# Performance work log

Hardware: AMD Instinct MI355X
Metric: run time of the kernel (lower is better)

Reference implementation:

```python
import jax, jax.numpy as jnp
import numpy as np
from jax import lax

L, H, C, V, BLK = 6, 12, 768, 50257, 1024
B, T = 4, 1024
HD = C // H
EPS = 1e-5


def _norm(key, shape, scale=0.02):
    return jax.random.normal(key, shape, dtype=jnp.float32) * scale


def setup_inputs() -> dict:
    key = jax.random.key(0)
    ks = jax.random.split(key, 16)
    idx = jax.random.randint(ks[0], (B, T), 0, V)
    inp = {
        "idx": idx,
        "wte": _norm(ks[1], (V, C)),
        "wpe": _norm(ks[2], (BLK, C)),
        "ln1_s": jnp.ones((L, C)),
        "ln1_b": jnp.zeros((L, C)),
        "qkv_w": _norm(ks[3], (L, C, 3 * C)),
        "qkv_b": jnp.zeros((L, 3 * C)),
        "proj_w": _norm(ks[4], (L, C, C)),
        "proj_b": jnp.zeros((L, C)),
        "ln2_s": jnp.ones((L, C)),
        "ln2_b": jnp.zeros((L, C)),
        "fc_w": _norm(ks[5], (L, C, 4 * C)),
        "fc_b": jnp.zeros((L, 4 * C)),
        "fcp_w": _norm(ks[6], (L, 4 * C, C)),
        "fcp_b": jnp.zeros((L, C)),
        "lnf_s": jnp.ones((C,)),
        "lnf_b": jnp.zeros((C,)),
    }
    return inp


def layer_norm(x, s, b):
    mu = jnp.mean(x, axis=-1, keepdims=True)
    var = jnp.mean(jnp.square(x - mu), axis=-1, keepdims=True)
    return (x - mu) * lax.rsqrt(var + EPS) * s + b


def block(x, p):
    ln1_s, ln1_b, qkv_w, qkv_b, proj_w, proj_b, ln2_s, ln2_b, fc_w, fc_b, fcp_w, fcp_b = p
    Bx, Tx, Cx = x.shape
    h = layer_norm(x, ln1_s, ln1_b)
    qkv = h @ qkv_w + qkv_b  # [B,T,3C]
    q, k, v = jnp.split(qkv, 3, axis=-1)
    q = q.reshape(Bx, Tx, H, HD).swapaxes(1, 2)  # [B,H,T,hd]
    k = k.reshape(Bx, Tx, H, HD).swapaxes(1, 2)
    v = v.reshape(Bx, Tx, H, HD).swapaxes(1, 2)
    attn = jnp.einsum("bhqd,bhkd->bhqk", q, k) / jnp.sqrt(jnp.float32(HD))
    mask = jnp.tril(jnp.ones((Tx, Tx), dtype=bool))
    attn = jnp.where(mask, attn, -jnp.inf)
    attn = jax.nn.softmax(attn, axis=-1)
    y = jnp.einsum("bhqk,bhkd->bhqd", attn, v)
    y = y.swapaxes(1, 2).reshape(Bx, Tx, Cx)
    x = x + (y @ proj_w + proj_b)
    h = layer_norm(x, ln2_s, ln2_b)
    h = jax.nn.gelu(h @ fc_w + fc_b, approximate=True)
    x = x + (h @ fcp_w + fcp_b)
    return x


def reference(idx, wte, wpe, ln1_s, ln1_b, qkv_w, qkv_b, proj_w, proj_b,
              ln2_s, ln2_b, fc_w, fc_b, fcp_w, fcp_b, lnf_s, lnf_b):
    Tx = idx.shape[1]
    x = wte[idx] + wpe[:Tx][None]  # [B,T,C]
    params = (ln1_s, ln1_b, qkv_w, qkv_b, proj_w, proj_b,
              ln2_s, ln2_b, fc_w, fc_b, fcp_w, fcp_b)
    def step(carry, p):
        return block(carry, p), None
    x, _ = lax.scan(step, x, params)
    x = layer_norm(x, lnf_s, lnf_b)
    logits = x @ wte.T  # tied embedding attend
    return logits
```

## Files before the change

kernel.cpp:

```cpp
#include <hip/hip_runtime.h>
#include <math.h>

#define LNUM 6
#define HNUM 12
#define CDIM 768
#define VDIM 50257
#define BDIM 4
#define TDIM 1024
#define NTOK 4096

typedef __bf16 bf16;
typedef __bf16 bf16x8 __attribute__((ext_vector_type(8)));
typedef float  floatx4 __attribute__((ext_vector_type(4)));
typedef unsigned int u32;

__device__ inline void gload16(const bf16* gsrc, bf16* lds) {
  __builtin_amdgcn_global_load_lds(
      (const __attribute__((address_space(1))) u32*)gsrc,
      (__attribute__((address_space(3))) u32*)lds, 16, 0, 0);
}

__global__ void k_cvt_bf16(const float* __restrict__ in, bf16* __restrict__ out, long n) {
  long i = ((long)blockIdx.x * blockDim.x + threadIdx.x) * 4;
  long stride = (long)gridDim.x * blockDim.x * 4;
  for (; i < n; i += stride) {
    float4 v = *reinterpret_cast<const float4*>(in + i);
    bf16 b0 = (bf16)v.x, b1 = (bf16)v.y, b2 = (bf16)v.z, b3 = (bf16)v.w;
    ushort4 pk;
    pk.x = __builtin_bit_cast(unsigned short, b0);
    pk.y = __builtin_bit_cast(unsigned short, b1);
    pk.z = __builtin_bit_cast(unsigned short, b2);
    pk.w = __builtin_bit_cast(unsigned short, b3);
    *reinterpret_cast<ushort4*>(out + i) = pk;
  }
}

__global__ void k_transpose_cvt(const float* __restrict__ in, bf16* __restrict__ out, int K, int N) {
  __shared__ float tile[32][33];
  int n0 = blockIdx.x * 32, k0 = blockIdx.y * 32;
  int nx = threadIdx.x & 31, ty = threadIdx.x >> 5;
  #pragma unroll
  for (int p = 0; p < 4; ++p) {
    int k = ty + p * 8;
    tile[k][nx] = in[(size_t)(k0 + k) * N + n0 + nx];
  }
  __syncthreads();
  #pragma unroll
  for (int p = 0; p < 4; ++p) {
    int n = ty + p * 8;
    out[(size_t)(n0 + n) * K + k0 + nx] = (bf16)tile[nx][n];
  }
}

__global__ void k_embed(const int* __restrict__ idx, const float* __restrict__ wte,
                        const float* __restrict__ wpe, float* __restrict__ x) {
  int tok = blockIdx.x;
  int t = tok & (TDIM - 1);
  int id = idx[tok];
  const float* a = wte + (size_t)id * CDIM;
  const float* p = wpe + (size_t)t * CDIM;
  float* o = x + (size_t)tok * CDIM;
  for (int c = threadIdx.x; c < CDIM; c += 256) o[c] = a[c] + p[c];
}

__global__ __launch_bounds__(256) void k_layernorm(const float* __restrict__ x,
    const float* __restrict__ sc, const float* __restrict__ bi, bf16* __restrict__ out) {
  __shared__ float red[8];
  int row = blockIdx.x;
  const float* xr = x + (size_t)row * CDIM;
  int t = threadIdx.x;
  float v0 = xr[t], v1 = xr[t + 256], v2 = xr[t + 512];
  float s = v0 + v1 + v2;
  #pragma unroll
  for (int o = 32; o > 0; o >>= 1) s += __shfl_down(s, o);
  if ((t & 63) == 0) red[t >> 6] = s;
  __syncthreads();
  float mean = (red[0] + red[1] + red[2] + red[3]) * (1.0f / CDIM);
  float d0 = v0 - mean, d1 = v1 - mean, d2 = v2 - mean;
  float q = d0 * d0 + d1 * d1 + d2 * d2;
  #pragma unroll
  for (int o = 32; o > 0; o >>= 1) q += __shfl_down(q, o);
  if ((t & 63) == 0) red[4 + (t >> 6)] = q;
  __syncthreads();
  float var = (red[4] + red[5] + red[6] + red[7]) * (1.0f / CDIM);
  float rs = rsqrtf(var + 1e-5f);
  bf16* orow = out + (size_t)row * CDIM;
  orow[t]       = (bf16)(d0 * rs * sc[t]       + bi[t]);
  orow[t + 256] = (bf16)(d1 * rs * sc[t + 256] + bi[t + 256]);
  orow[t + 512] = (bf16)(d2 * rs * sc[t + 512] + bi[t + 512]);
}

__device__ inline float gelu_f(float x) {
  float x3 = x * x * x;
  return 0.5f * x * (1.0f + tanhf(0.7978845608028654f * (x + 0.044715f * x3)));
}

template<int EPI>
__global__ __launch_bounds__(512, 1) void k_gemm8(
    const bf16* __restrict__ A, const bf16* __restrict__ Bt,
    const float* __restrict__ bias,
    float* __restrict__ Cf, bf16* __restrict__ Cb,
    int N, int K) {
  __shared__ __align__(16) bf16 lds[2][4][8192];
  const int nwg = gridDim.x;
  const int id = blockIdx.x;
  const int swz = (id & 7) * (nwg >> 3) + (id >> 3);
  const int m0 = (swz & 15) * 256;
  const int n0 = (swz >> 4) * 256;
  const int tid = threadIdx.x, lane = tid & 63, wave = tid >> 6;
  const int wr = wave >> 2, wc = wave & 3;
  const int g = lane >> 4, r16 = lane & 15;
  const int numK = K >> 6;

  const int srow = wave * 16 + (lane >> 2);
  const int scol = (lane & 3) * 8;
  const bf16* aptr0 = A  + (size_t)(m0 + srow) * K + scol;
  const bf16* aptr1 = A  + (size_t)(m0 + srow + 128) * K + scol;
  const bf16* bptr0 = Bt + (size_t)(n0 + srow) * K + scol;
  const bf16* bptr1 = Bt + (size_t)(n0 + srow + 128) * K + scol;
  const int a_off = (wr * 128 + r16) * 32 + g * 8;
  const int b_off = (wc * 64 + r16) * 32 + g * 8;

  floatx4 acc[8][4] = {};

#define STAGE_HALF(H) do {                                                \
    int H_ = (H);                                                         \
    if (H_ < numK * 4) {                                                  \
      int tau_ = H_ >> 2, h_ = H_ & 3;                                    \
      int isA_ = (h_ & 1), kk_ = (h_ >> 1) & 1;                           \
      bf16* dst_ = &lds[tau_ & 1][h_][wave * 512];                        \
      int ko_ = tau_ * 64 + kk_ * 32;                                     \
      gload16((isA_ ? aptr0 : bptr0) + ko_, dst_);                        \
      gload16((isA_ ? aptr1 : bptr1) + ko_, dst_ + 4096);                 \
    } } while (0)

  STAGE_HALF(0); STAGE_HALF(1); STAGE_HALF(2); STAGE_HALF(3);
  STAGE_HALF(4); STAGE_HALF(5); STAGE_HALF(6);
  asm volatile("s_waitcnt vmcnt(6)" ::: "memory");
  __builtin_amdgcn_s_barrier();

  for (int t = 0; t < numK; ++t) {
    const int p = t & 1;
    const int Hb = 4 * t + 7;
    bf16x8 af[4], bfr[4];

    #pragma unroll
    for (int j = 0; j < 4; ++j) bfr[j] = *(const bf16x8*)&lds[p][0][b_off + j * 512];
    #pragma unroll
    for (int i = 0; i < 4; ++i) af[i] = *(const bf16x8*)&lds[p][1][a_off + i * 512];
    STAGE_HALF(Hb);
    __builtin_amdgcn_s_barrier();
    asm volatile("s_waitcnt lgkmcnt(0)" ::: "memory");
    __builtin_amdgcn_s_setprio(1);
    #pragma unroll
    for (int i = 0; i < 4; ++i)
      #pragma unroll
      for (int j = 0; j < 4; ++j)
        acc[i][j] = __builtin_amdgcn_mfma_f32_16x16x32_bf16(af[i], bfr[j], acc[i][j], 0, 0, 0);
    __builtin_amdgcn_s_setprio(0);
    __builtin_amdgcn_s_barrier();

    #pragma unroll
    for (int i = 0; i < 4; ++i) af[i] = *(const bf16x8*)&lds[p][1][a_off + (i + 4) * 512];
    STAGE_HALF(Hb + 1);
    __builtin_amdgcn_s_barrier();
    asm volatile("s_waitcnt lgkmcnt(0)" ::: "memory");
    __builtin_amdgcn_s_setprio(1);
    #pragma unroll
    for (int i = 0; i < 4; ++i)
      #pragma unroll
      for (int j = 0; j < 4; ++j)
        acc[i + 4][j] = __builtin_amdgcn_mfma_f32_16x16x32_bf16(af[i], bfr[j], acc[i + 4][j], 0, 0, 0);
    __builtin_amdgcn_s_setprio(0);
    __builtin_amdgcn_s_barrier();

    #pragma unroll
    for (int j = 0; j < 4; ++j) bfr[j] = *(const bf16x8*)&lds[p][2][b_off + j * 512];
    #pragma unroll
    for (int i = 0; i < 4; ++i) af[i] = *(const bf16x8*)&lds[p][3][a_off + i * 512];
    STAGE_HALF(Hb + 2);
    __builtin_amdgcn_s_barrier();
    asm volatile("s_waitcnt lgkmcnt(0)" ::: "memory");
    __builtin_amdgcn_s_setprio(1);
    #pragma unroll
    for (int i = 0; i < 4; ++i)
      #pragma unroll
      for (int j = 0; j < 4; ++j)
        acc[i][j] = __builtin_amdgcn_mfma_f32_16x16x32_bf16(af[i], bfr[j], acc[i][j], 0, 0, 0);
    __builtin_amdgcn_s_setprio(0);
    __builtin_amdgcn_s_barrier();

    #pragma unroll
    for (int i = 0; i < 4; ++i) af[i] = *(const bf16x8*)&lds[p][3][a_off + (i + 4) * 512];
    STAGE_HALF(Hb + 3);
    __builtin_amdgcn_s_barrier();
    asm volatile("s_waitcnt lgkmcnt(0)" ::: "memory");
    __builtin_amdgcn_s_setprio(1);
    #pragma unroll
    for (int i = 0; i < 4; ++i)
      #pragma unroll
      for (int j = 0; j < 4; ++j)
        acc[i + 4][j] = __builtin_amdgcn_mfma_f32_16x16x32_bf16(af[i], bfr[j], acc[i + 4][j], 0, 0, 0);
    __builtin_amdgcn_s_setprio(0);
    if (t + 2 < numK) { asm volatile("s_waitcnt vmcnt(6)" ::: "memory"); }
    else              { asm volatile("s_waitcnt vmcnt(0)" ::: "memory"); }
    __builtin_amdgcn_s_barrier();
  }
#undef STAGE_HALF

  const int mb = m0 + wr * 128 + g * 4;
  const int nb = n0 + wc * 64 + r16;
  #pragma unroll
  for (int nf = 0; nf < 4; ++nf) {
    int n = nb + nf * 16;
    if (EPI == 0 && n >= N) continue;
    float bv = (EPI >= 3) ? bias[n] : 0.0f;
    #pragma unroll
    for (int mf = 0; mf < 8; ++mf) {
      #pragma unroll
      for (int q = 0; q < 4; ++q) {
        int m = mb + mf * 16 + q;
        float v = acc[mf][nf][q] + bv;
        size_t o = (size_t)m * N + n;
        if (EPI == 3)      Cb[o] = (bf16)gelu_f(v);
        else if (EPI == 4) Cb[o] = (bf16)v;
        else               Cf[o] = v;
      }
    }
  }
}

template<int TBM, int MI, int NI, int EPI>
__global__ __launch_bounds__(256) void k_gemm(
    const bf16* __restrict__ A, const bf16* __restrict__ Bt,
    const float* __restrict__ bias, const float* __restrict__ resid,
    float* __restrict__ Cf, bf16* __restrict__ Cb,
    int M, int N, int K) {
  constexpr int BN = 128;
  constexpr int WGN = BN / (NI * 16);
  constexpr int AI = TBM / 32;
  constexpr int BI = BN / 32;
  __shared__ __align__(16) bf16 As[TBM * 64];
  __shared__ __align__(16) bf16 Bs[BN * 64];
  const int m0 = blockIdx.x * TBM, n0 = blockIdx.y * BN;
  const int tid = threadIdx.x;
  const int lane = tid & 63, wave = tid >> 6;
  const int wr = wave / WGN, wc = wave % WGN;
  const int l8 = lane >> 3, s8 = lane & 7;
  const int g = lane >> 4, r16 = lane & 15;

  floatx4 acc[MI][NI] = {};

  const bf16* a_src = A + (size_t)(m0 + l8) * K + s8 * 8;
  const bf16* b_src = Bt + (size_t)(n0 + l8) * K + s8 * 8;

  for (int k0 = 0; k0 < K; k0 += 64) {
    #pragma unroll
    for (int t = 0; t < AI; ++t) {
      int row0 = wave * (TBM / 4) + t * 8;
      gload16(a_src + (size_t)row0 * K + k0, &As[row0 * 64]);
    }
    #pragma unroll
    for (int t = 0; t < BI; ++t) {
      int row0 = wave * 32 + t * 8;
      gload16(b_src + (size_t)row0 * K + k0, &Bs[row0 * 64]);
    }
    __syncthreads();
    #pragma unroll
    for (int kk = 0; kk < 2; ++kk) {
      bf16x8 af[MI], bfr[NI];
      #pragma unroll
      for (int i = 0; i < MI; ++i)
        af[i] = *reinterpret_cast<const bf16x8*>(&As[(wr * MI * 16 + i * 16 + r16) * 64 + g * 8 + kk * 32]);
      #pragma unroll
      for (int j = 0; j < NI; ++j)
        bfr[j] = *reinterpret_cast<const bf16x8*>(&Bs[(wc * NI * 16 + j * 16 + r16) * 64 + g * 8 + kk * 32]);
      #pragma unroll
      for (int i = 0; i < MI; ++i) {
        #pragma unroll
        for (int j = 0; j < NI; ++j)
          acc[i][j] = __builtin_amdgcn_mfma_f32_16x16x32_bf16(af[i], bfr[j], acc[i][j], 0, 0, 0);
      }
    }
    __syncthreads();
  }

  int mb = m0 + wr * MI * 16 + g * 4;
  int nb = n0 + wc * NI * 16 + r16;
  #pragma unroll
  for (int j = 0; j < NI; ++j) {
    int n = nb + j * 16;
    if (n >= N) continue;
    float bv = (EPI >= 2) ? bias[n] : 0.0f;
    #pragma unroll
    for (int i = 0; i < MI; ++i) {
      #pragma unroll
      for (int q = 0; q < 4; ++q) {
        int m = mb + i * 16 + q;
        float v = acc[i][j][q] + bv;
        size_t o = (size_t)m * N + n;
        if (EPI == 2)      Cf[o] = v + resid[o];
        else if (EPI == 3) Cb[o] = (bf16)gelu_f(v);
        else if (EPI == 4) Cb[o] = (bf16)v;
        else               Cf[o] = v;
      }
    }
  }
}

__global__ __launch_bounds__(256) void k_vtrans(const bf16* __restrict__ qkv, bf16* __restrict__ vt) {
  __shared__ bf16 tile[64][72];
  int bh = blockIdx.x, t0 = blockIdx.y * 64;
  int b = bh / HNUM, h = bh % HNUM;
  int tid = threadIdx.x;
  int r8 = tid >> 3, s8 = tid & 7;
  #pragma unroll
  for (int p = 0; p < 2; ++p) {
    int row = p * 32 + r8;
    uint4 v = *reinterpret_cast<const uint4*>(
        qkv + (size_t)(b * TDIM + t0 + row) * (3 * CDIM) + 2 * CDIM + h * 64 + s8 * 8);
    *reinterpret_cast<uint4*>(&tile[row][s8 * 8]) = v;
  }
  __syncthreads();
  int d = tid >> 2, q4 = tid & 3;
  #pragma unroll
  for (int half = 0; half < 2; ++half) {
    int t = q4 * 16 + half * 8;
    bf16x8 o;
    #pragma unroll
    for (int u = 0; u < 8; ++u) o[u] = tile[t + u][d];
    *reinterpret_cast<bf16x8*>(vt + (size_t)bh * (64 * TDIM) + (size_t)d * TDIM + t0 + t) = o;
  }
}

__global__ __launch_bounds__(256) void k_attn(const bf16* __restrict__ qkv,
                                              const bf16* __restrict__ vt,
                                              bf16* __restrict__ y) {
  __shared__ __align__(16) bf16 Ks[64 * 64];
  __shared__ __align__(16) bf16 Vs[64 * 64];
  __shared__ __align__(16) bf16 Ps[64 * 64];
  const int bh = blockIdx.x, qt = blockIdx.y;
  const int b = bh / HNUM, h = bh % HNUM;
  const int tid = threadIdx.x, lane = tid & 63, wave = tid >> 6;
  const int g = lane >> 4, r16 = lane & 15;
  const int w16 = wave * 16;
  const int r8 = tid >> 3, s8 = tid & 7;

  bf16x8 qf[2];
  {
    const bf16* qsrc = qkv + (size_t)(b * TDIM + qt * 64 + w16 + r16) * (3 * CDIM) + h * 64 + g * 8;
    qf[0] = *reinterpret_cast<const bf16x8*>(qsrc);
    qf[1] = *reinterpret_cast<const bf16x8*>(qsrc + 32);
  }

  float m_r[4], l_r[4];
  floatx4 yacc[4] = {};
  #pragma unroll
  for (int q = 0; q < 4; ++q) { m_r[q] = -1e30f; l_r[q] = 0.f; }

  for (int kt = 0; kt <= qt; ++kt) {
    __syncthreads();
    #pragma unroll
    for (int p = 0; p < 2; ++p) {
      int row = p * 32 + r8;
      uint4 kv = *reinterpret_cast<const uint4*>(
          qkv + (size_t)(b * TDIM + kt * 64 + row) * (3 * CDIM) + CDIM + h * 64 + s8 * 8);
      *reinterpret_cast<uint4*>(&Ks[row * 64 + ((s8 ^ (row & 7)) * 8)]) = kv;
      uint4 vv = *reinterpret_cast<const uint4*>(
          vt + (size_t)bh * (64 * TDIM) + (size_t)row * TDIM + kt * 64 + s8 * 8);
      *reinterpret_cast<uint4*>(&Vs[row * 64 + ((s8 ^ (row & 7)) * 8)]) = vv;
    }
    __syncthreads();

    floatx4 sa[4] = {};
    #pragma unroll
    for (int c = 0; c < 2; ++c) {
      bf16x8 kf[4];
      #pragma unroll
      for (int j = 0; j < 4; ++j) {
        int krow = j * 16 + r16;
        kf[j] = *reinterpret_cast<const bf16x8*>(&Ks[krow * 64 + (((g + 4 * c) ^ (krow & 7)) * 8)]);
      }
      #pragma unroll
      for (int j = 0; j < 4; ++j)
        sa[j] = __builtin_amdgcn_mfma_f32_16x16x32_bf16(qf[c], kf[j], sa[j], 0, 0, 0);
    }

    const bool diag = (kt == qt);
    float p_v[4][4];
    #pragma unroll
    for (int q = 0; q < 4; ++q) {
      int qrow = w16 + g * 4 + q;
      float mx = -1e30f;
      #pragma unroll
      for (int j = 0; j < 4; ++j) {
        float s = sa[j][q] * 0.125f;
        if (diag && (r16 + j * 16) > qrow) s = -1e30f;
        p_v[j][q] = s;
        mx = fmaxf(mx, s);
      }
      #pragma unroll
      for (int o = 1; o < 16; o <<= 1) mx = fmaxf(mx, __shfl_xor(mx, o));
      float mnew = fmaxf(m_r[q], mx);
      float ps = 0.f;
      #pragma unroll
      for (int j = 0; j < 4; ++j) {
        float p = __expf(p_v[j][q] - mnew);
        p_v[j][q] = p;
        ps += p;
      }
      #pragma unroll
      for (int o = 1; o < 16; o <<= 1) ps += __shfl_xor(ps, o);
      float alpha = __expf(m_r[q] - mnew);
      m_r[q] = mnew;
      l_r[q] = l_r[q] * alpha + ps;
      #pragma unroll
      for (int j = 0; j < 4; ++j) yacc[j][q] *= alpha;
      #pragma unroll
      for (int j = 0; j < 4; ++j) {
        int col = r16 + j * 16;
        Ps[qrow * 64 + (col ^ ((qrow & 7) << 3))] = (bf16)p_v[j][q];
      }
    }

    #pragma unroll
    for (int ks = 0; ks < 2; ++ks) {
      int prow = w16 + r16;
      bf16x8 pa = *reinterpret_cast<const bf16x8*>(&Ps[prow * 64 + (((g + 4 * ks) ^ (prow & 7)) * 8)]);
      #pragma unroll
      for (int j = 0; j < 4; ++j) {
        int vrow = j * 16 + r16;
        bf16x8 vb = *reinterpret_cast<const bf16x8*>(&Vs[vrow * 64 + (((g + 4 * ks) ^ (vrow & 7)) * 8)]);
        yacc[j] = __builtin_amdgcn_mfma_f32_16x16x32_bf16(pa, vb, yacc[j], 0, 0, 0);
      }
    }
  }

  #pragma unroll
  for (int q = 0; q < 4; ++q) {
    float inv = 1.0f / l_r[q];
    int tok = b * TDIM + qt * 64 + w16 + g * 4 + q;
    #pragma unroll
    for (int j = 0; j < 4; ++j)
      y[(size_t)tok * CDIM + h * 64 + r16 + j * 16] = (bf16)(yacc[j][q] * inv);
  }
}

extern "C" void kernel_launch(void* const* d_in, const int* in_sizes, int n_in,
                              void* d_out, int out_size, void* d_ws, size_t ws_size,
                              hipStream_t stream) {
  (void)in_sizes; (void)n_in; (void)out_size;
  const int*   idx    = (const int*)  d_in[0];
  const float* wte    = (const float*)d_in[1];
  const float* wpe    = (const float*)d_in[2];
  const float* ln1_s  = (const float*)d_in[3];
  const float* ln1_b  = (const float*)d_in[4];
  const float* qkv_w  = (const float*)d_in[5];
  const float* qkv_b  = (const float*)d_in[6];
  const float* proj_w = (const float*)d_in[7];
  const float* proj_b = (const float*)d_in[8];
  const float* ln2_s  = (const float*)d_in[9];
  const float* ln2_b  = (const float*)d_in[10];
  const float* fc_w   = (const float*)d_in[11];
  const float* fc_b   = (const float*)d_in[12];
  const float* fcp_w  = (const float*)d_in[13];
  const float* fcp_b  = (const float*)d_in[14];
  const float* lnf_s  = (const float*)d_in[15];
  const float* lnf_b  = (const float*)d_in[16];
  float* logits = (float*)d_out;

  char* base = (char*)d_ws;
  size_t off = 0;
  auto alloc = [&](size_t bytes) -> void* {
    void* p = base + off;
    off += (bytes + 255) & ~(size_t)255;
    return p;
  };
  bf16*  wte_bf = (bf16*) alloc((size_t)VDIM * CDIM * 2);
  bf16*  wq_t   = (bf16*) alloc((size_t)3 * CDIM * CDIM * 2);
  bf16*  wp_t   = (bf16*) alloc((size_t)CDIM * CDIM * 2);
  bf16*  wf_t   = (bf16*) alloc((size_t)4 * CDIM * CDIM * 2);
  bf16*  wfp_t  = (bf16*) alloc((size_t)4 * CDIM * CDIM * 2);
  float* x      = (float*)alloc((size_t)NTOK * CDIM * 4);
  bf16*  hb     = (bf16*) alloc((size_t)NTOK * CDIM * 2);
  bf16*  qkv_bf = (bf16*) alloc((size_t)NTOK * 3 * CDIM * 2);
  bf16*  vt     = (bf16*) alloc((size_t)BDIM * HNUM * 64 * TDIM * 2);
  bf16*  yb     = (bf16*) alloc((size_t)NTOK * CDIM * 2);
  bf16*  gb     = (bf16*) alloc((size_t)NTOK * 4 * CDIM * 2);
  if (off > ws_size) return;

  k_cvt_bf16<<<4096, 256, 0, stream>>>(wte, wte_bf, (long)VDIM * CDIM);
  k_embed<<<NTOK, 256, 0, stream>>>(idx, wte, wpe, x);

  for (int l = 0; l < LNUM; ++l) {
    k_transpose_cvt<<<dim3(3*CDIM/32, CDIM/32), 256, 0, stream>>>(qkv_w + (size_t)l*CDIM*3*CDIM, wq_t, CDIM, 3*CDIM);
    k_transpose_cvt<<<dim3(CDIM/32,   CDIM/32), 256, 0, stream>>>(proj_w + (size_t)l*CDIM*CDIM,  wp_t, CDIM, CDIM);
    k_transpose_cvt<<<dim3(4*CDIM/32, CDIM/32), 256, 0, stream>>>(fc_w  + (size_t)l*CDIM*4*CDIM, wf_t, CDIM, 4*CDIM);
    k_transpose_cvt<<<dim3(CDIM/32, 4*CDIM/32), 256, 0, stream>>>(fcp_w + (size_t)l*4*CDIM*CDIM, wfp_t, 4*CDIM, CDIM);

    k_layernorm<<<NTOK, 256, 0, stream>>>(x, ln1_s + l*CDIM, ln1_b + l*CDIM, hb);
    k_gemm8<4><<<16 * 9, 512, 0, stream>>>(hb, wq_t, qkv_b + (size_t)l*3*CDIM, nullptr, qkv_bf, 3*CDIM, CDIM);
    k_vtrans<<<dim3(BDIM*HNUM, TDIM/64), 256, 0, stream>>>(qkv_bf, vt);
    k_attn<<<dim3(BDIM*HNUM, TDIM/64), 256, 0, stream>>>(qkv_bf, vt, yb);
    k_gemm<64,4,2,2><<<dim3(NTOK/64, 6), 256, 0, stream>>>(yb, wp_t, proj_b + (size_t)l*CDIM, x, x, nullptr, NTOK, CDIM, CDIM);
    k_layernorm<<<NTOK, 256, 0, stream>>>(x, ln2_s + l*CDIM, ln2_b + l*CDIM, hb);
    k_gemm8<3><<<16 * 12, 512, 0, stream>>>(hb, wf_t, fc_b + (size_t)l*4*CDIM, nullptr, gb, 4*CDIM, CDIM);
    k_gemm<64,4,2,2><<<dim3(NTOK/64, 6), 256, 0, stream>>>(gb, wfp_t, fcp_b + (size_t)l*CDIM, x, x, nullptr, NTOK, CDIM, 4*CDIM);
  }

  k_layernorm<<<NTOK, 256, 0, stream>>>(x, lnf_s, lnf_b, hb);
  int ntile = (VDIM + 255) / 256;
  k_gemm8<0><<<16 * ntile, 512, 0, stream>>>(hb, wte_bf, nullptr, logits, nullptr, VDIM, CDIM);
}
```

Measured before the change: 2.049 ms.

## Batch weight transposes into one launch and stage GEMM epilogue through LDS

Replaces the 24 per-layer weight transpose/convert launches with one kernel that converts all layers' weights up front into per-layer buffers. In the big GEMM, the staging macro gives way to pointer-increment loads, and the logits epilogue switches to nontemporal fp32 stores. The bf16 epilogues now go through LDS so each row is written with 16-byte vector stores instead of scattered 2-byte stores. In exchange the workspace grows to hold all six layers' weights.

```diff
diff --git a/kernel.cpp b/kernel.cpp
--- a/kernel.cpp
+++ b/kernel.cpp
@@ -35,20 +35,49 @@
   }
 }
 
-__global__ void k_transpose_cvt(const float* __restrict__ in, bf16* __restrict__ out, int K, int N) {
+#define TILES_QKV  1728
+#define TILES_PROJ 576
+#define TILES_FC   2304
+#define TILES_FCP  2304
+#define TILES_LAYER (TILES_QKV + TILES_PROJ + TILES_FC + TILES_FCP)
+
+__global__ __launch_bounds__(256) void k_trans_all(
+    const float* __restrict__ qkv_w, const float* __restrict__ proj_w,
+    const float* __restrict__ fc_w, const float* __restrict__ fcp_w,
+    bf16* __restrict__ wq, bf16* __restrict__ wp,
+    bf16* __restrict__ wf, bf16* __restrict__ wfp) {
   __shared__ float tile[32][33];
-  int n0 = blockIdx.x * 32, k0 = blockIdx.y * 32;
-  int nx = threadIdx.x & 31, ty = threadIdx.x >> 5;
+  int bid = blockIdx.x;
+  int layer = bid / TILES_LAYER, r = bid % TILES_LAYER;
+  const float* src; bf16* dst; int K, N, tx, ty;
+  if (r < TILES_QKV) {
+    src = qkv_w + (size_t)layer * CDIM * 3 * CDIM; dst = wq + (size_t)layer * CDIM * 3 * CDIM;
+    K = CDIM; N = 3 * CDIM; tx = r % 72; ty = r / 72;
+  } else if (r < TILES_QKV + TILES_PROJ) {
+    r -= TILES_QKV;
+    src = proj_w + (size_t)layer * CDIM * CDIM; dst = wp + (size_t)layer * CDIM * CDIM;
+    K = CDIM; N = CDIM; tx = r % 24; ty = r / 24;
+  } else if (r < TILES_QKV + TILES_PROJ + TILES_FC) {
+    r -= TILES_QKV + TILES_PROJ;
+    src = fc_w + (size_t)layer * CDIM * 4 * CDIM; dst = wf + (size_t)layer * CDIM * 4 * CDIM;
+    K = CDIM; N = 4 * CDIM; tx = r % 96; ty = r / 96;
+  } else {
+    r -= TILES_QKV + TILES_PROJ + TILES_FC;
+    src = fcp_w + (size_t)layer * 4 * CDIM * CDIM; dst = wfp + (size_t)layer * 4 * CDIM * CDIM;
+    K = 4 * CDIM; N = CDIM; tx = r % 24; ty = r / 24;
+  }
+  int n0 = tx * 32, k0 = ty * 32;
+  int nx = threadIdx.x & 31, tyy = threadIdx.x >> 5;
   #pragma unroll
   for (int p = 0; p < 4; ++p) {
-    int k = ty + p * 8;
-    tile[k][nx] = in[(size_t)(k0 + k) * N + n0 + nx];
+    int k = tyy + p * 8;
+    tile[k][nx] = src[(size_t)(k0 + k) * N + n0 + nx];
   }
   __syncthreads();
   #pragma unroll
   for (int p = 0; p < 4; ++p) {
-    int n = ty + p * 8;
-    out[(size_t)(n0 + n) * K + k0 + nx] = (bf16)tile[nx][n];
+    int n = tyy + p * 8;
+    dst[(size_t)(n0 + n) * K + k0 + nx] = (bf16)tile[nx][n];
   }
 }
 
@@ -111,44 +140,40 @@
   const int wr = wave >> 2, wc = wave & 3;
   const int g = lane >> 4, r16 = lane & 15;
   const int numK = K >> 6;
+  const int wsl = wave * 512;
 
   const int srow = wave * 16 + (lane >> 2);
   const int scol = (lane & 3) * 8;
-  const bf16* aptr0 = A  + (size_t)(m0 + srow) * K + scol;
-  const bf16* aptr1 = A  + (size_t)(m0 + srow + 128) * K + scol;
-  const bf16* bptr0 = Bt + (size_t)(n0 + srow) * K + scol;
-  const bf16* bptr1 = Bt + (size_t)(n0 + srow + 128) * K + scol;
+  const bf16* at  = A  + (size_t)(m0 + srow) * K + scol;
+  const bf16* at1 = A  + (size_t)(m0 + srow + 128) * K + scol;
+  const bf16* bt  = Bt + (size_t)(n0 + srow) * K + scol;
+  const bf16* bt1 = Bt + (size_t)(n0 + srow + 128) * K + scol;
   const int a_off = (wr * 128 + r16) * 32 + g * 8;
   const int b_off = (wc * 64 + r16) * 32 + g * 8;
 
   floatx4 acc[8][4] = {};
 
-#define STAGE_HALF(H) do {                                                \
-    int H_ = (H);                                                         \
-    if (H_ < numK * 4) {                                                  \
-      int tau_ = H_ >> 2, h_ = H_ & 3;                                    \
-      int isA_ = (h_ & 1), kk_ = (h_ >> 1) & 1;                           \
-      bf16* dst_ = &lds[tau_ & 1][h_][wave * 512];                        \
-      int ko_ = tau_ * 64 + kk_ * 32;                                     \
-      gload16((isA_ ? aptr0 : bptr0) + ko_, dst_);                        \
-      gload16((isA_ ? aptr1 : bptr1) + ko_, dst_ + 4096);                 \
-    } } while (0)
-
-  STAGE_HALF(0); STAGE_HALF(1); STAGE_HALF(2); STAGE_HALF(3);
-  STAGE_HALF(4); STAGE_HALF(5); STAGE_HALF(6);
+#define G2(sA, sB, dst) do { gload16((sA), (dst)); gload16((sB), (dst) + 4096); } while (0)
+
+  G2(bt,      bt1,      &lds[0][0][wsl]);
+  G2(at,      at1,      &lds[0][1][wsl]);
+  G2(bt + 32, bt1 + 32, &lds[0][2][wsl]);
+  G2(at + 32, at1 + 32, &lds[0][3][wsl]);
+  G2(bt + 64, bt1 + 64, &lds[1][0][wsl]);
+  G2(at + 64, at1 + 64, &lds[1][1][wsl]);
+  G2(bt + 96, bt1 + 96, &lds[1][2][wsl]);
   asm volatile("s_waitcnt vmcnt(6)" ::: "memory");
   __builtin_amdgcn_s_barrier();
 
   for (int t = 0; t < numK; ++t) {
-    const int p = t & 1;
-    const int Hb = 4 * t + 7;
+    const int p = t & 1, pn = p ^ 1;
     bf16x8 af[4], bfr[4];
 
     #pragma unroll
     for (int j = 0; j < 4; ++j) bfr[j] = *(const bf16x8*)&lds[p][0][b_off + j * 512];
     #pragma unroll
     for (int i = 0; i < 4; ++i) af[i] = *(const bf16x8*)&lds[p][1][a_off + i * 512];
-    STAGE_HALF(Hb);
+    if (t + 1 < numK) G2(at + 96, at1 + 96, &lds[pn][3][wsl]);
     __builtin_amdgcn_s_barrier();
     asm volatile("s_waitcnt lgkmcnt(0)" ::: "memory");
     __builtin_amdgcn_s_setprio(1);
@@ -162,7 +187,7 @@
 
     #pragma unroll
     for (int i = 0; i < 4; ++i) af[i] = *(const bf16x8*)&lds[p][1][a_off + (i + 4) * 512];
-    STAGE_HALF(Hb + 1);
+    if (t + 2 < numK) G2(bt + 128, bt1 + 128, &lds[p][0][wsl]);
     __builtin_amdgcn_s_barrier();
     asm volatile("s_waitcnt lgkmcnt(0)" ::: "memory");
     __builtin_amdgcn_s_setprio(1);
@@ -178,7 +203,7 @@
     for (int j = 0; j < 4; ++j) bfr[j] = *(const bf16x8*)&lds[p][2][b_off + j * 512];
     #pragma unroll
     for (int i = 0; i < 4; ++i) af[i] = *(const bf16x8*)&lds[p][3][a_off + i * 512];
-    STAGE_HALF(Hb + 2);
+    if (t + 2 < numK) G2(at + 128, at1 + 128, &lds[p][1][wsl]);
     __builtin_amdgcn_s_barrier();
     asm volatile("s_waitcnt lgkmcnt(0)" ::: "memory");
     __builtin_amdgcn_s_setprio(1);
@@ -192,7 +217,7 @@
 
     #pragma unroll
     for (int i = 0; i < 4; ++i) af[i] = *(const bf16x8*)&lds[p][3][a_off + (i + 4) * 512];
-    STAGE_HALF(Hb + 3);
+    if (t + 2 < numK) G2(bt + 160, bt1 + 160, &lds[p][2][wsl]);
     __builtin_amdgcn_s_barrier();
     asm volatile("s_waitcnt lgkmcnt(0)" ::: "memory");
     __builtin_amdgcn_s_setprio(1);
@@ -205,27 +230,50 @@
     if (t + 2 < numK) { asm volatile("s_waitcnt vmcnt(6)" ::: "memory"); }
     else              { asm volatile("s_waitcnt vmcnt(0)" ::: "memory"); }
     __builtin_amdgcn_s_barrier();
-  }
-#undef STAGE_HALF
-
-  const int mb = m0 + wr * 128 + g * 4;
-  const int nb = n0 + wc * 64 + r16;
-  #pragma unroll
-  for (int nf = 0; nf < 4; ++nf) {
-    int n = nb + nf * 16;
-    if (EPI == 0 && n >= N) continue;
-    float bv = (EPI >= 3) ? bias[n] : 0.0f;
+
+    at += 64; at1 += 64; bt += 64; bt1 += 64;
+  }
+#undef G2
+
+  if (EPI == 0) {
+    const int mb = m0 + wr * 128 + g * 4;
+    const int nb = n0 + wc * 64 + r16;
+    #pragma unroll
+    for (int nf = 0; nf < 4; ++nf) {
+      int n = nb + nf * 16;
+      if (n >= N) continue;
+      #pragma unroll
+      for (int mf = 0; mf < 8; ++mf) {
+        #pragma unroll
+        for (int q = 0; q < 4; ++q) {
+          int m = mb + mf * 16 + q;
+          __builtin_nontemporal_store(acc[mf][nf][q], &Cf[(size_t)m * N + n]);
+        }
+      }
+    }
+  } else {
+    bf16* sb = &lds[0][0][0] + wave * 1152;
+    const int rr_rd = lane & 15, seg = lane >> 4;
+    const int nb = n0 + wc * 64 + r16;
+    float bv[4];
+    #pragma unroll
+    for (int j = 0; j < 4; ++j) bv[j] = bias[nb + j * 16];
     #pragma unroll
     for (int mf = 0; mf < 8; ++mf) {
       #pragma unroll
-      for (int q = 0; q < 4; ++q) {
-        int m = mb + mf * 16 + q;
-        float v = acc[mf][nf][q] + bv;
-        size_t o = (size_t)m * N + n;
-        if (EPI == 3)      Cb[o] = (bf16)gelu_f(v);
-        else if (EPI == 4) Cb[o] = (bf16)v;
-        else               Cf[o] = v;
-      }
+      for (int j = 0; j < 4; ++j) {
+        #pragma unroll
+        for (int q = 0; q < 4; ++q) {
+          float v = acc[mf][j][q] + bv[j];
+          if (EPI == 3) v = gelu_f(v);
+          sb[(g * 4 + q) * 72 + j * 16 + r16] = (bf16)v;
+        }
+      }
+      bf16x8 o0 = *(const bf16x8*)&sb[rr_rd * 72 + seg * 16];
+      bf16x8 o1 = *(const bf16x8*)&sb[rr_rd * 72 + seg * 16 + 8];
+      size_t orow = (size_t)(m0 + wr * 128 + mf * 16 + rr_rd) * N + (n0 + wc * 64 + seg * 16);
+      *(bf16x8*)&Cb[orow] = o0;
+      *(bf16x8*)&Cb[orow + 8] = o1;
     }
   }
 }
@@ -476,36 +524,38 @@
     off += (bytes + 255) & ~(size_t)255;
     return p;
   };
-  bf16*  wte_bf = (bf16*) alloc((size_t)VDIM * CDIM * 2);
-  bf16*  wq_t   = (bf16*) alloc((size_t)3 * CDIM * CDIM * 2);
-  bf16*  wp_t   = (bf16*) alloc((size_t)CDIM * CDIM * 2);
-  bf16*  wf_t   = (bf16*) alloc((size_t)4 * CDIM * CDIM * 2);
-  bf16*  wfp_t  = (bf16*) alloc((size_t)4 * CDIM * CDIM * 2);
-  float* x      = (float*)alloc((size_t)NTOK * CDIM * 4);
-  bf16*  hb     = (bf16*) alloc((size_t)NTOK * CDIM * 2);
-  bf16*  qkv_bf = (bf16*) alloc((size_t)NTOK * 3 * CDIM * 2);
-  bf16*  vt     = (bf16*) alloc((size_t)BDIM * HNUM * 64 * TDIM * 2);
-  bf16*  yb     = (bf16*) alloc((size_t)NTOK * CDIM * 2);
-  bf16*  gb     = (bf16*) alloc((size_t)NTOK * 4 * CDIM * 2);
+  bf16*  wte_bf  = (bf16*) alloc((size_t)VDIM * CDIM * 2);
+  bf16*  wq_all  = (bf16*) alloc((size_t)LNUM * 3 * CDIM * CDIM * 2);
+  bf16*  wp_all  = (bf16*) alloc((size_t)LNUM * CDIM * CDIM * 2);
+  bf16*  wf_all  = (bf16*) alloc((size_t)LNUM * 4 * CDIM * CDIM * 2);
+  bf16*  wfp_all = (bf16*) alloc((size_t)LNUM * 4 * CDIM * CDIM * 2);
+  float* x       = (float*)alloc((size_t)NTOK * CDIM * 4);
+  bf16*  hb      = (bf16*) alloc((size_t)NTOK * CDIM * 2);
+  bf16*  qkv_bf  = (bf16*) alloc((size_t)NTOK * 3 * CDIM * 2);
+  bf16*  vt      = (bf16*) alloc((size_t)BDIM * HNUM * 64 * TDIM * 2);
+  bf16*  yb      = (bf16*) alloc((size_t)NTOK * CDIM * 2);
+  bf16*  gb      = (bf16*) alloc((size_t)NTOK * 4 * CDIM * 2);
   if (off > ws_size) return;
 
   k_cvt_bf16<<<4096, 256, 0, stream>>>(wte, wte_bf, (long)VDIM * CDIM);
+  k_trans_all<<<LNUM * TILES_LAYER, 256, 0, stream>>>(qkv_w, proj_w, fc_w, fcp_w,
+                                                      wq_all, wp_all, wf_all, wfp_all);
   k_embed<<<NTOK, 256, 0, stream>>>(idx, wte, wpe, x);
 
   for (int l = 0; l < LNUM; ++l) {
-    k_transpose_cvt<<<dim3(3*CDIM/32, CDIM/32), 256, 0, stream>>>(qkv_w + (size_t)l*CDIM*3*CDIM, wq_t, CDIM, 3*CDIM);
-    k_transpose_cvt<<<dim3(CDIM/32,   CDIM/32), 256, 0, stream>>>(proj_w + (size_t)l*CDIM*CDIM,  wp_t, CDIM, CDIM);
-    k_transpose_cvt<<<dim3(4*CDIM/32, CDIM/32), 256, 0, stream>>>(fc_w  + (size_t)l*CDIM*4*CDIM, wf_t, CDIM, 4*CDIM);
-    k_transpose_cvt<<<dim3(CDIM/32, 4*CDIM/32), 256, 0, stream>>>(fcp_w + (size_t)l*4*CDIM*CDIM, wfp_t, 4*CDIM, CDIM);
+    const bf16* wq  = wq_all  + (size_t)l * 3 * CDIM * CDIM;
+    const bf16* wp  = wp_all  + (size_t)l * CDIM * CDIM;
+    const bf16* wf  = wf_all  + (size_t)l * 4 * CDIM * CDIM;
+    const bf16* wfp = wfp_all + (size_t)l * 4 * CDIM * CDIM;
 
     k_layernorm<<<NTOK, 256, 0, stream>>>(x, ln1_s + l*CDIM, ln1_b + l*CDIM, hb);
-    k_gemm8<4><<<16 * 9, 512, 0, stream>>>(hb, wq_t, qkv_b + (size_t)l*3*CDIM, nullptr, qkv_bf, 3*CDIM, CDIM);
+    k_gemm8<4><<<16 * 9, 512, 0, stream>>>(hb, wq, qkv_b + (size_t)l*3*CDIM, nullptr, qkv_bf, 3*CDIM, CDIM);
     k_vtrans<<<dim3(BDIM*HNUM, TDIM/64), 256, 0, stream>>>(qkv_bf, vt);
     k_attn<<<dim3(BDIM*HNUM, TDIM/64), 256, 0, stream>>>(qkv_bf, vt, yb);
-    k_gemm<64,4,2,2><<<dim3(NTOK/64, 6), 256, 0, stream>>>(yb, wp_t, proj_b + (size_t)l*CDIM, x, x, nullptr, NTOK, CDIM, CDIM);
+    k_gemm<64,4,2,2><<<dim3(NTOK/64, 6), 256, 0, stream>>>(yb, wp, proj_b + (size_t)l*CDIM, x, x, nullptr, NTOK, CDIM, CDIM);
     k_layernorm<<<NTOK, 256, 0, stream>>>(x, ln2_s + l*CDIM, ln2_b + l*CDIM, hb);
-    k_gemm8<3><<<16 * 12, 512, 0, stream>>>(hb, wf_t, fc_b + (size_t)l*4*CDIM, nullptr, gb, 4*CDIM, CDIM);
-    k_gemm<64,4,2,2><<<dim3(NTOK/64, 6), 256, 0, stream>>>(gb, wfp_t, fcp_b + (size_t)l*CDIM, x, x, nullptr, NTOK, CDIM, 4*CDIM);
+    k_gemm8<3><<<16 * 12, 512, 0, stream>>>(hb, wf, fc_b + (size_t)l*4*CDIM, nullptr, gb, 4*CDIM, CDIM);
+    k_gemm<64,4,2,2><<<dim3(NTOK/64, 6), 256, 0, stream>>>(gb, wfp, fcp_b + (size_t)l*CDIM, x, x, nullptr, NTOK, CDIM, 4*CDIM);
   }
 
   k_layernorm<<<NTOK, 256, 0, stream>>>(x, lnf_s, lnf_b, hb);
```

New measurement: 2.319 ms. 13.2% more time.
